# Optimization experiments

Measured on AMD Instinct MI355X. Metric: run time of the kernel, lower is better.

Reference implementation:

```python
import jax, jax.numpy as jnp
import numpy as np

B, T, N, F = 8, 12, 10000, 8
H = 64          # hidden_size
K = 2           # diffusion hops (gnn_kernel)
HOR = 12        # horizon
E = 320000      # num edges


def setup_inputs() -> dict:
    key = jax.random.key(0)
    ks = jax.random.split(key, 12)
    s = 0.1  # param scale
    return {
        "x": jax.random.normal(ks[0], (B, T, N, F), jnp.float32),
        "edge_index": jax.random.randint(ks[1], (2, E), 0, N, jnp.int64),
        "edge_weight": jax.random.uniform(ks[2], (E,), jnp.float32),
        "enc_W": jax.random.normal(ks[3], (F, H), jnp.float32) * s,
        "enc_b": jnp.zeros((H,), jnp.float32),
        "node_emb": jax.random.normal(ks[4], (N, H), jnp.float32) * s,
        "Wih": jax.random.normal(ks[5], (3 * H, H), jnp.float32) * s,
        "Whh": jax.random.normal(ks[6], (3 * H, H), jnp.float32) * s,
        "bih": jnp.zeros((3 * H,), jnp.float32),
        "bhh": jnp.zeros((3 * H,), jnp.float32),
        "filt_W": jax.random.normal(ks[7], (H * (2 * K + 1), H), jnp.float32) * s,
        "filt_b": jnp.zeros((H,), jnp.float32),
        "dec_W": jax.random.normal(ks[8], (H, F * HOR), jnp.float32) * s,
        "dec_b": jnp.zeros((F * HOR,), jnp.float32),
    }


def _gru_last(xs, Wih, Whh, bih, bhh):
    # xs: [T, M, H] -> last hidden state [M, H]; torch GRU gate order r,z,n
    gx = jnp.einsum('tmh,gh->tmg', xs, Wih) + bih  # [T, M, 3H]
    h0 = jnp.zeros(xs.shape[1:], xs.dtype)

    def step(h, gxt):
        gh = h @ Whh.T + bhh
        xr, xz, xn = jnp.split(gxt, 3, -1)
        hr, hz, hn = jnp.split(gh, 3, -1)
        r = jax.nn.sigmoid(xr + hr)
        z = jax.nn.sigmoid(xz + hz)
        n = jnp.tanh(xn + r * hn)
        return (1.0 - z) * n + z * h, None

    h, _ = jax.lax.scan(step, h0, gx)
    return h


def _diff_conv(h, edge_index, edge_weight, W, b):
    # h: [B, N, H]; diffusion conv with forward + backward transition matrices
    src, tgt = edge_index[0], edge_index[1]

    def prop(x, s, t, w):
        deg = jax.ops.segment_sum(w, t, num_segments=N)      # in-degree of aggregating node
        nw = w / jnp.where(deg[t] == 0, 1.0, deg[t])
        msg = x[:, s, :] * nw[None, :, None]                 # [B, E, H]
        return jnp.zeros_like(x).at[:, t].add(msg)

    outs = [h]  # root weight
    for s, t in ((src, tgt), (tgt, src)):  # forward then backward diffusion
        z = h
        for _ in range(K):
            z = prop(z, s, t, edge_weight)
            outs.append(z)
    return jnp.concatenate(outs, axis=-1) @ W + b


def reference(x, edge_index, edge_weight, enc_W, enc_b, node_emb, Wih, Whh,
              bih, bhh, filt_W, filt_b, dec_W, dec_b):
    x_enc = x @ enc_W + enc_b                         # [B,T,N,H]
    x_emb = x_enc + node_emb                          # broadcast over B,T
    xs = jnp.transpose(x_emb, (1, 0, 2, 3)).reshape(T, B * N, H)
    h = _gru_last(xs, Wih, Whh, bih, bhh).reshape(B, N, H)
    z = _diff_conv(h, edge_index, edge_weight, filt_W, filt_b)
    x_out = z @ dec_W + dec_b                         # [B,N,F*HOR]
    x_hor = x_out.reshape(B, N, HOR, F).transpose(0, 2, 1, 3)  # b t n f
    return x_hor
```

## Files before the change

### kernel.cpp

```cpp
#include <hip/hip_runtime.h>

typedef unsigned short ushort_t;

#define NN 10000
#define BB 8
#define TT 12
#define FF 8
#define HH 64
#define GG 192
#define HORZ 12
#define EE 320000
#define MM (BB*NN)

#define NL2E (-1.4426950408889634f)
#define P2L2E (2.8853900817779268f)

#define OFF_H    0u
#define OFF_F1   5120000u
#define OFF_F2   10240000u
#define OFF_B1   15360000u
#define OFF_B2   20480000u
#define OFF_BIAS 25600000u
#define OFF_W1   27520000u
#define OFF_DEGF 27521536u
#define OFF_DEGB 27531536u
#define OFF_CNTF 27541536u
#define OFF_CNTB 27551536u
#define OFF_PTRF 27561536u
#define OFF_PTRB 27571537u
#define OFF_EPKF 27581538u
#define OFF_EPKB 28221538u
#define OFF_FLAG 28861538u

typedef __attribute__((ext_vector_type(8))) short short8;
typedef __attribute__((ext_vector_type(4))) float f4v;

union I4S8 { int4 i; short8 s; };

__device__ __forceinline__ f4v mfma16(int4 a, int4 b, f4v c) {
    I4S8 ua, ub; ua.i = a; ub.i = b;
    return __builtin_amdgcn_mfma_f32_16x16x32_bf16(ua.s, ub.s, c, 0, 0, 0);
}

__device__ __forceinline__ unsigned f2bf_u(float f) {
    union { float f; unsigned u; } v; v.f = f;
    unsigned x = v.u;
    x += 0x7FFFu + ((x >> 16) & 1u);
    return x >> 16;
}
__device__ __forceinline__ int4 hi8(const float* f) {
    unsigned hb[8];
    #pragma unroll
    for (int i = 0; i < 8; i++) hb[i] = f2bf_u(f[i]);
    return make_int4((int)(hb[0]|(hb[1]<<16)), (int)(hb[2]|(hb[3]<<16)),
                     (int)(hb[4]|(hb[5]<<16)), (int)(hb[6]|(hb[7]<<16)));
}

__device__ __forceinline__ float f4c(const float4& v, int kk) {
    switch (kk) { case 0: return v.x; case 1: return v.y; case 2: return v.z; default: return v.w; }
}
#define FMA4(ACC, W, S) \
    ACC[0] = fmaf(S, W.x, ACC[0]); \
    ACC[1] = fmaf(S, W.y, ACC[1]); \
    ACC[2] = fmaf(S, W.z, ACC[2]); \
    ACC[3] = fmaf(S, W.w, ACC[3]);

__global__ void zero_k(float* p, int n) {
    int i = blockIdx.x * 256 + threadIdx.x;
    if (i < n) p[i] = 0.f;
}

__global__ void flag_k(const int* __restrict__ ei, int* flag) {
    if (threadIdx.x == 0 && blockIdx.x == 0) {
        int o = ei[1] | ei[3] | ei[5] | ei[7] | ei[9] | ei[11] | ei[13];
        flag[0] = (o == 0) ? 1 : 0;
    }
}

__device__ __forceinline__ void load_edge(const int* __restrict__ ei, int isI64,
                                          int e, int& s, int& t) {
    if (isI64) {
        const long long* p = (const long long*)ei;
        s = (int)p[e]; t = (int)p[EE + e];
    } else {
        s = ei[e]; t = ei[EE + e];
    }
}

__global__ void csr_count_k(const int* __restrict__ ei, const float* __restrict__ ew,
                            const int* __restrict__ flag,
                            int* cnt_f, int* cnt_b, float* deg_f, float* deg_b) {
    int e = blockIdx.x * 256 + threadIdx.x;
    if (e >= EE) return;
    int isI64 = flag[0];
    int s, t; load_edge(ei, isI64, e, s, t);
    if ((unsigned)s >= NN || (unsigned)t >= NN) return;
    float w = ew[e];
    atomicAdd(&cnt_f[t], 1); atomicAdd(&deg_f[t], w);
    atomicAdd(&cnt_b[s], 1); atomicAdd(&deg_b[s], w);
}

__global__ void scan_k(int* cnt_f, int* cnt_b, int* ptr_f, int* ptr_b) {
    int* cnt = blockIdx.x ? cnt_b : cnt_f;
    int* ptr = blockIdx.x ? ptr_b : ptr_f;
    __shared__ int part[256];
    int tid = threadIdx.x;
    const int CH = (NN + 255) / 256;
    int lo = tid * CH, hi = lo + CH; if (hi > NN) hi = NN; if (lo > NN) lo = NN;
    int s = 0;
    for (int i = lo; i < hi; i++) s += cnt[i];
    part[tid] = s;
    __syncthreads();
    if (tid == 0) {
        int run = 0;
        for (int i = 0; i < 256; i++) { int v = part[i]; part[i] = run; run += v; }
        ptr[NN] = run;
    }
    __syncthreads();
    int run = part[tid];
    for (int i = lo; i < hi; i++) { ptr[i] = run; run += cnt[i]; cnt[i] = 0; }
}

__global__ void csr_fill_k(const int* __restrict__ ei, const float* __restrict__ ew,
                           const int* __restrict__ flag,
                           const float* __restrict__ deg_f, const float* __restrict__ deg_b,
                           const int* __restrict__ ptr_f, const int* __restrict__ ptr_b,
                           int* cnt_f, int* cnt_b,
                           int* epk_f, int* epk_b) {
    int e = blockIdx.x * 256 + threadIdx.x;
    if (e >= EE) return;
    int isI64 = flag[0];
    int s, t; load_edge(ei, isI64, e, s, t);
    if ((unsigned)s >= NN || (unsigned)t >= NN) return;
    float w = ew[e];
    float df = deg_f[t];
    float nwf = w / ((df == 0.f) ? 1.f : df);
    int p = ptr_f[t] + atomicAdd(&cnt_f[t], 1);
    epk_f[2 * p] = s; epk_f[2 * p + 1] = __float_as_int(nwf);
    float db = deg_b[s];
    float nwb = w / ((db == 0.f) ? 1.f : db);
    int p2 = ptr_b[s] + atomicAdd(&cnt_b[s], 1);
    epk_b[2 * p2] = t; epk_b[2 * p2 + 1] = __float_as_int(nwb);
}

__global__ void w1_k(const float* __restrict__ encW, const float* __restrict__ wih,
                     float* __restrict__ W1) {
    int id = blockIdx.x * 256 + threadIdx.x;
    if (id >= FF * GG) return;
    int f = id / GG, g = id - f * GG;
    float acc = 0.f;
    for (int hh = 0; hh < HH; hh++)
        acc = fmaf(encW[f * HH + hh], wih[g * HH + hh], acc);
    W1[id] = acc * ((g < 128) ? NL2E : P2L2E);
}

__global__ __launch_bounds__(256, 2)
void biasA_k(const float* __restrict__ emb, const float* __restrict__ encb,
             const float* __restrict__ wih, const float* __restrict__ bih,
             const float* __restrict__ bhh, float* __restrict__ biasA) {
    __shared__ float wl[HH * GG];
    __shared__ float et[64 * 68];
    const int tid = threadIdx.x;
    const int n0 = blockIdx.x * 64;
    for (int idx = tid * 4; idx < GG * HH; idx += 1024) {
        float4 v = *(const float4*)&wih[idx];
        int g = idx >> 6, hh = idx & 63;
        wl[hh * GG + g] = v.x;
        wl[(hh + 1) * GG + g] = v.y;
        wl[(hh + 2) * GG + g] = v.z;
        wl[(hh + 3) * GG + g] = v.w;
    }
    {
        int row = tid >> 2, cc = (tid & 3) * 16;
        int n = n0 + row;
        #pragma unroll
        for (int u = 0; u < 4; u++) {
            float4 e4 = (n < NN) ? *(const float4*)&emb[(size_t)n * HH + cc + u * 4]
                                 : make_float4(0.f, 0.f, 0.f, 0.f);
            float4 b4 = *(const float4*)&encb[cc + u * 4];
            *(float4*)&et[row * 68 + cc + u * 4] =
                make_float4(e4.x + b4.x, e4.y + b4.y, e4.z + b4.z, e4.w + b4.w);
        }
    }
    __syncthreads();
    const int r0 = (tid >> 4) * 4;
    #pragma unroll 1
    for (int p = 0; p < 3; p++) {
        const int c0 = p * 64 + (tid & 15) * 4;
        float acc[4][4];
        float4 bi = *(const float4*)&bih[c0];
        float4 bh = (c0 < 128) ? *(const float4*)&bhh[c0] : make_float4(0.f, 0.f, 0.f, 0.f);
        #pragma unroll
        for (int i = 0; i < 4; i++) {
            acc[i][0] = bi.x + bh.x; acc[i][1] = bi.y + bh.y;
            acc[i][2] = bi.z + bh.z; acc[i][3] = bi.w + bh.w;
        }
        #pragma unroll 4
        for (int k4 = 0; k4 < 64; k4 += 4) {
            float4 hv[4];
            #pragma unroll
            for (int i = 0; i < 4; i++)
                hv[i] = *(const float4*)&et[(r0 + i) * 68 + k4];
            #pragma unroll
            for (int kk = 0; kk < 4; kk++) {
                const float4 wv = *(const float4*)&wl[(k4 + kk) * GG + c0];
                #pragma unroll
                for (int i = 0; i < 4; i++) {
                    float a_ = f4c(hv[i], kk);
                    FMA4(acc[i], wv, a_);
                }
            }
        }
        #pragma unroll
        for (int i = 0; i < 4; i++) {
            int n = n0 + r0 + i;
            if (n < NN)
                *(float4*)&biasA[(size_t)n * GG + c0] =
                    make_float4(acc[i][0], acc[i][1], acc[i][2], acc[i][3]);
        }
    }
}

__global__ __launch_bounds__(256, 2)
void gru_k(const float* __restrict__ x, const float* __restrict__ biasA,
           const float* __restrict__ W1, const float* __restrict__ whh,
           const float* __restrict__ bhh, float* __restrict__ h_out) {
    __shared__ int lds_B[24 * 64 * 4];
    __shared__ int lds_W1[12 * 64 * 4];
    __shared__ __align__(16) ushort_t lds_hb[4][16 * 68];

    const int tid = threadIdx.x;
    const int wave = tid >> 6, ln = tid & 63;
    const int quad = ln >> 4, lx = ln & 15;
    const int m0 = blockIdx.x * 64;
    ushort_t* hbw = (ushort_t*)lds_hb[wave];

    #pragma unroll
    for (int it = 0; it < 6; it++) {
        int slot = tid + it * 256;
        int fid = slot >> 6, l2 = slot & 63;
        int c = fid >> 1, q = fid & 1;
        int g = c * 16 + (l2 & 15);
        int k0 = q * 32 + ((l2 >> 4) & 3) * 8;
        float sc = (c < 8) ? NL2E : P2L2E;
        const float* wp = whh + (size_t)g * HH + k0;
        float4 v0 = *(const float4*)wp;
        float4 v1 = *(const float4*)(wp + 4);
        float fv[8] = {v0.x * sc, v0.y * sc, v0.z * sc, v0.w * sc,
                       v1.x * sc, v1.y * sc, v1.z * sc, v1.w * sc};
        *(int4*)&lds_B[slot * 4] = hi8(fv);
    }

    #pragma unroll
    for (int it = 0; it < 3; it++) {
        int slot = tid + it * 256;
        int f = slot >> 6, l2 = slot & 63;
        int4 v = make_int4(0, 0, 0, 0);
        if (l2 < 16) {
            int col = f * 16 + l2;
            float fv[8];
            #pragma unroll
            for (int k = 0; k < 8; k++) fv[k] = W1[k * GG + col];
            v = hi8(fv);
        }
        *(int4*)&lds_W1[slot * 4] = v;
    }

    f4v bR[4], bZ[4], bNx[4];
    float bHn[4];
    int rown[4];
    #pragma unroll
    for (int reg = 0; reg < 4; reg++) {
        int m = m0 + wave * 16 + quad * 4 + reg;
        int b = m / NN; rown[reg] = m - b * NN;
    }
    #pragma unroll
    for (int j = 0; j < 4; j++) {
        int c = j * 16 + lx;
        #pragma unroll
        for (int reg = 0; reg < 4; reg++) {
            const float* bp = biasA + (size_t)rown[reg] * GG;
            bR[j][reg]  = bp[c] * NL2E;
            bZ[j][reg]  = bp[64 + c] * NL2E;
            bNx[j][reg] = bp[128 + c] * P2L2E;
        }
        bHn[j] = bhh[128 + c] * P2L2E;
    }

    const float* xp = x;
    float4 xc0 = make_float4(0.f,0.f,0.f,0.f), xc1 = xc0;
    if (ln < 16) {
        int m = m0 + wave * 16 + ln;
        int b = m / NN; int n = m - b * NN;
        xp = x + ((size_t)(b * TT) * NN + n) * FF;
        xc0 = *(const float4*)xp;
        xc1 = *(const float4*)(xp + 4);
    }

    __syncthreads();

    f4v hp[4];
    #pragma unroll
    for (int j = 0; j < 4; j++) hp[j] = (f4v){0.f, 0.f, 0.f, 0.f};

    #pragma unroll 1
    for (int t = 0; t < TT; t++) {
        int4 axh = make_int4(0, 0, 0, 0);
        {
            float fv[8] = {xc0.x, xc0.y, xc0.z, xc0.w, xc1.x, xc1.y, xc1.z, xc1.w};
            if (ln < 16) axh = hi8(fv);
        }
        if (t < TT - 1 && ln < 16) {
            const float* xq = xp + (size_t)(t + 1) * (NN * FF);
            xc0 = *(const float4*)xq;
            xc1 = *(const float4*)(xq + 4);
        }

        int4 ahf[2];
        if (t) {
            const ushort_t* h0 = hbw + lx * 68 + quad * 8;
            long long a00, a01, a10, a11;
            __builtin_memcpy(&a00, h0, 8);
            __builtin_memcpy(&a01, h0 + 4, 8);
            __builtin_memcpy(&a10, h0 + 32, 8);
            __builtin_memcpy(&a11, h0 + 36, 8);
            ahf[0] = make_int4((int)a00, (int)(a00 >> 32), (int)a01, (int)(a01 >> 32));
            ahf[1] = make_int4((int)a10, (int)(a10 >> 32), (int)a11, (int)(a11 >> 32));
        }

        f4v accR[4], accZ[4], accNx[4], accNh[4];
        #pragma unroll
        for (int j = 0; j < 4; j++) {
            int4 wR = *(const int4*)&lds_W1[((j    ) * 64 + ln) * 4];
            int4 wZ = *(const int4*)&lds_W1[((j + 4) * 64 + ln) * 4];
            int4 wN = *(const int4*)&lds_W1[((j + 8) * 64 + ln) * 4];
            accR[j]  = mfma16(axh, wR, bR[j]);
            accZ[j]  = mfma16(axh, wZ, bZ[j]);
            accNx[j] = mfma16(axh, wN, bNx[j]);
            accNh[j] = (f4v){bHn[j], bHn[j], bHn[j], bHn[j]};
        }
        if (t) {
            #pragma unroll
            for (int j = 0; j < 4; j++) {
                #pragma unroll
                for (int q = 0; q < 2; q++) {
                    int4 bRf = *(const int4*)&lds_B[((j * 2 + q) * 64 + ln) * 4];
                    int4 bZf = *(const int4*)&lds_B[(((j + 4) * 2 + q) * 64 + ln) * 4];
                    int4 bNf = *(const int4*)&lds_B[(((j + 8) * 2 + q) * 64 + ln) * 4];
                    accR[j]  = mfma16(ahf[q], bRf, accR[j]);
                    accZ[j]  = mfma16(ahf[q], bZf, accZ[j]);
                    accNh[j] = mfma16(ahf[q], bNf, accNh[j]);
                }
            }
        }

        #pragma unroll
        for (int j = 0; j < 4; j++) {
            #pragma unroll
            for (int reg = 0; reg < 4; reg++) {
                float rr = __builtin_amdgcn_rcpf(1.f + __builtin_amdgcn_exp2f(accR[j][reg]));
                float zz = __builtin_amdgcn_rcpf(1.f + __builtin_amdgcn_exp2f(accZ[j][reg]));
                float pre = fmaf(rr, accNh[j][reg], accNx[j][reg]);
                float e2 = __builtin_amdgcn_exp2f(pre);
                float nn = fmaf(-2.f, __builtin_amdgcn_rcpf(e2 + 1.f), 1.f);
                float hv = fmaf(zz, hp[j][reg] - nn, nn);
                hp[j][reg] = hv;
                hbw[(quad * 4 + reg) * 68 + j * 16 + lx] = (ushort_t)f2bf_u(hv);
            }
        }
    }

    #pragma unroll
    for (int j = 0; j < 4; j++) {
        #pragma unroll
        for (int reg = 0; reg < 4; reg++) {
            int m = m0 + wave * 16 + quad * 4 + reg;
            h_out[(size_t)m * HH + j * 16 + lx] = hp[j][reg];
        }
    }
}

__global__ __launch_bounds__(128)
void prop_k(const float* __restrict__ srcF, float* __restrict__ dstF,
            const int* __restrict__ ptrF, const long long* __restrict__ epkF,
            const float* __restrict__ srcB, float* __restrict__ dstB,
            const int* __restrict__ ptrB, const long long* __restrict__ epkB) {
    const int wv = __builtin_amdgcn_readfirstlane(threadIdx.x >> 6);
    const int ln = threadIdx.x & 63;
    const int b = blockIdx.x & 7;
    const int node = (blockIdx.x >> 3) * 2 + wv;
    const float* src; float* dst; const int* ptr; const long long* ep;
    if (blockIdx.z == 0) { src = srcF; dst = dstF; ptr = ptrF; ep = epkF; }
    else                 { src = srcB; dst = dstB; ptr = ptrB; ep = epkB; }
    const int uoff = b * (NN * HH) + ln;
    const int e0 = ptr[node], e1 = ptr[node + 1];

    float a0 = 0.f, a1 = 0.f, a2 = 0.f, a3 = 0.f;
    float a4 = 0.f, a5 = 0.f, a6 = 0.f, a7 = 0.f;
    int j = e0;
    for (; j + 16 <= e1; j += 16) {
        long long r0 = ep[j + 0],  r1 = ep[j + 1],  r2 = ep[j + 2],  r3 = ep[j + 3];
        long long r4 = ep[j + 4],  r5 = ep[j + 5],  r6 = ep[j + 6],  r7 = ep[j + 7];
        long long r8 = ep[j + 8],  r9 = ep[j + 9],  rA = ep[j + 10], rB = ep[j + 11];
        long long rC = ep[j + 12], rD = ep[j + 13], rE = ep[j + 14], rF = ep[j + 15];
        float v0 = (src + ((size_t)(int)r0 << 6))[uoff];
        float v1 = (src + ((size_t)(int)r1 << 6))[uoff];
        float v2 = (src + ((size_t)(int)r2 << 6))[uoff];
        float v3 = (src + ((size_t)(int)r3 << 6))[uoff];
        float v4 = (src + ((size_t)(int)r4 << 6))[uoff];
        float v5 = (src + ((size_t)(int)r5 << 6))[uoff];
        float v6 = (src + ((size_t)(int)r6 << 6))[uoff];
        float v7 = (src + ((size_t)(int)r7 << 6))[uoff];
        float v8 = (src + ((size_t)(int)r8 << 6))[uoff];
        float v9 = (src + ((size_t)(int)r9 << 6))[uoff];
        float vA = (src + ((size_t)(int)rA << 6))[uoff];
        float vB = (src + ((size_t)(int)rB << 6))[uoff];
        float vC = (src + ((size_t)(int)rC << 6))[uoff];
        float vD = (src + ((size_t)(int)rD << 6))[uoff];
        float vE = (src + ((size_t)(int)rE << 6))[uoff];
        float vF = (src + ((size_t)(int)rF << 6))[uoff];
        a0 = fmaf(v0, __int_as_float((int)(r0 >> 32)), a0);
        a1 = fmaf(v1, __int_as_float((int)(r1 >> 32)), a1);
        a2 = fmaf(v2, __int_as_float((int)(r2 >> 32)), a2);
        a3 = fmaf(v3, __int_as_float((int)(r3 >> 32)), a3);
        a4 = fmaf(v4, __int_as_float((int)(r4 >> 32)), a4);
        a5 = fmaf(v5, __int_as_float((int)(r5 >> 32)), a5);
        a6 = fmaf(v6, __int_as_float((int)(r6 >> 32)), a6);
        a7 = fmaf(v7, __int_as_float((int)(r7 >> 32)), a7);
        a0 = fmaf(v8, __int_as_float((int)(r8 >> 32)), a0);
        a1 = fmaf(v9, __int_as_float((int)(r9 >> 32)), a1);
        a2 = fmaf(vA, __int_as_float((int)(rA >> 32)), a2);
        a3 = fmaf(vB, __int_as_float((int)(rB >> 32)), a3);
        a4 = fmaf(vC, __int_as_float((int)(rC >> 32)), a4);
        a5 = fmaf(vD, __int_as_float((int)(rD >> 32)), a5);
        a6 = fmaf(vE, __int_as_float((int)(rE >> 32)), a6);
        a7 = fmaf(vF, __int_as_float((int)(rF >> 32)), a7);
    }
    for (; j + 8 <= e1; j += 8) {
        long long r0 = ep[j + 0], r1 = ep[j + 1], r2 = ep[j + 2], r3 = ep[j + 3];
        long long r4 = ep[j + 4], r5 = ep[j + 5], r6 = ep[j + 6], r7 = ep[j + 7];
        float v0 = (src + ((size_t)(int)r0 << 6))[uoff];
        float v1 = (src + ((size_t)(int)r1 << 6))[uoff];
        float v2 = (src + ((size_t)(int)r2 << 6))[uoff];
        float v3 = (src + ((size_t)(int)r3 << 6))[uoff];
        float v4 = (src + ((size_t)(int)r4 << 6))[uoff];
        float v5 = (src + ((size_t)(int)r5 << 6))[uoff];
        float v6 = (src + ((size_t)(int)r6 << 6))[uoff];
        float v7 = (src + ((size_t)(int)r7 << 6))[uoff];
        a0 = fmaf(v0, __int_as_float((int)(r0 >> 32)), a0);
        a1 = fmaf(v1, __int_as_float((int)(r1 >> 32)), a1);
        a2 = fmaf(v2, __int_as_float((int)(r2 >> 32)), a2);
        a3 = fmaf(v3, __int_as_float((int)(r3 >> 32)), a3);
        a4 = fmaf(v4, __int_as_float((int)(r4 >> 32)), a4);
        a5 = fmaf(v5, __int_as_float((int)(r5 >> 32)), a5);
        a6 = fmaf(v6, __int_as_float((int)(r6 >> 32)), a6);
        a7 = fmaf(v7, __int_as_float((int)(r7 >> 32)), a7);
    }
    for (; j < e1; j++) {
        long long r0 = ep[j];
        a0 = fmaf((src + ((size_t)(int)r0 << 6))[uoff],
                  __int_as_float((int)(r0 >> 32)), a0);
    }
    float s = ((a0 + a1) + (a2 + a3)) + ((a4 + a5) + (a6 + a7));
    __builtin_nontemporal_store(s, &dst[((size_t)b * NN + node) * HH + ln]);
}

__global__ __launch_bounds__(256, 2)
void filtdec_k(const float* __restrict__ h, const float* __restrict__ f1,
               const float* __restrict__ f2, const float* __restrict__ b1,
               const float* __restrict__ b2,
               const float* __restrict__ filtW, const float* __restrict__ filtb,
               const float* __restrict__ decW, const float* __restrict__ decb,
               float* __restrict__ out) {
    __shared__ float lds_a[64 * 100];
    __shared__ float lds_w[64 * 100];
    const int tid = threadIdx.x;
    const int m0 = blockIdx.x * 64;
    const int c0 = (tid & 15) * 4, r0 = (tid >> 4) * 4;

    float acc[4][4];
    #pragma unroll
    for (int i = 0; i < 4; i++)
        #pragma unroll
        for (int j = 0; j < 4; j++) acc[i][j] = 0.f;

    #pragma unroll 1
    for (int q = 0; q < 5; q++) {
        const float* src = (q == 0) ? h : (q == 1) ? f1 : (q == 2) ? f2 : (q == 3) ? b1 : b2;
        {
            int row = tid >> 2, cc = (tid & 3) * 16;
            const float* sp = src + (size_t)(m0 + row) * HH + cc;
            float4 v0 = *(const float4*)(sp + 0);
            float4 v1 = *(const float4*)(sp + 4);
            float4 v2 = *(const float4*)(sp + 8);
            float4 v3 = *(const float4*)(sp + 12);
            *(float4*)&lds_a[row * 100 + cc + 0]  = v0;
            *(float4*)&lds_a[row * 100 + cc + 4]  = v1;
            *(float4*)&lds_a[row * 100 + cc + 8]  = v2;
            *(float4*)&lds_a[row * 100 + cc + 12] = v3;
        }
        {
            int k = tid >> 2, cc = (tid & 3) * 16;
            const float* wp = filtW + (size_t)(q * 64 + k) * HH + cc;
            float4 v0 = *(const float4*)(wp + 0);
            float4 v1 = *(const float4*)(wp + 4);
            float4 v2 = *(const float4*)(wp + 8);
            float4 v3 = *(const float4*)(wp + 12);
            *(float4*)&lds_w[k * 100 + cc + 0]  = v0;
            *(float4*)&lds_w[k * 100 + cc + 4]  = v1;
            *(float4*)&lds_w[k * 100 + cc + 8]  = v2;
            *(float4*)&lds_w[k * 100 + cc + 12] = v3;
        }
        __syncthreads();
        #pragma unroll 4
        for (int k4 = 0; k4 < 64; k4 += 4) {
            float4 iv[4];
            #pragma unroll
            for (int i = 0; i < 4; i++)
                iv[i] = *(const float4*)&lds_a[(r0 + i) * 100 + k4];
            #pragma unroll
            for (int kk = 0; kk < 4; kk++) {
                const float4 wv = *(const float4*)&lds_w[(k4 + kk) * 100 + c0];
                #pragma unroll
                for (int i = 0; i < 4; i++) {
                    float a_ = f4c(iv[i], kk);
                    FMA4(acc[i], wv, a_);
                }
            }
        }
        __syncthreads();
    }
    {
        float fb[4];
        #pragma unroll
        for (int j = 0; j < 4; j++) fb[j] = filtb[c0 + j];
        #pragma unroll
        for (int i = 0; i < 4; i++)
            *(float4*)&lds_a[(r0 + i) * 68 + c0] =
                make_float4(acc[i][0] + fb[0], acc[i][1] + fb[1],
                            acc[i][2] + fb[2], acc[i][3] + fb[3]);
    }
    {
        int k = tid >> 2, cc = (tid & 3) * 24;
        const float* wp = decW + k * 96 + cc;
        float* dstp = &lds_w[k * 100 + cc];
        #pragma unroll
        for (int u = 0; u < 6; u++) {
            float4 v = *(const float4*)(wp + u * 4);
            *(float4*)(dstp + u * 4) = v;
        }
    }
    __syncthreads();

    const int c0b = (tid & 15) * 6;
    float acc2[4][6];
    #pragma unroll
    for (int i = 0; i < 4; i++)
        #pragma unroll
        for (int j = 0; j < 6; j++) acc2[i][j] = 0.f;
    #pragma unroll 4
    for (int k4 = 0; k4 < 64; k4 += 4) {
        float4 zv[4];
        #pragma unroll
        for (int i = 0; i < 4; i++)
            zv[i] = *(const float4*)&lds_a[(r0 + i) * 68 + k4];
        #pragma unroll
        for (int kk = 0; kk < 4; kk++) {
            float2 wa = *(const float2*)&lds_w[(k4 + kk) * 100 + c0b];
            float2 wb = *(const float2*)&lds_w[(k4 + kk) * 100 + c0b + 2];
            float2 wc = *(const float2*)&lds_w[(k4 + kk) * 100 + c0b + 4];
            #pragma unroll
            for (int i = 0; i < 4; i++) {
                float zz = f4c(zv[i], kk);
                acc2[i][0] = fmaf(zz, wa.x, acc2[i][0]);
                acc2[i][1] = fmaf(zz, wa.y, acc2[i][1]);
                acc2[i][2] = fmaf(zz, wb.x, acc2[i][2]);
                acc2[i][3] = fmaf(zz, wb.y, acc2[i][3]);
                acc2[i][4] = fmaf(zz, wc.x, acc2[i][4]);
                acc2[i][5] = fmaf(zz, wc.y, acc2[i][5]);
            }
        }
    }
    __syncthreads();
    {
        float db[6];
        #pragma unroll
        for (int j = 0; j < 6; j++) db[j] = decb[c0b + j];
        #pragma unroll
        for (int i = 0; i < 4; i++)
            #pragma unroll
            for (int j = 0; j < 6; j++)
                lds_w[(r0 + i) * 100 + c0b + j] = acc2[i][j] + db[j];
    }
    __syncthreads();
    #pragma unroll 1
    for (int hor = 0; hor < HORZ; hor++) {
        int nl = tid >> 2, fp = tid & 3;
        int m = m0 + nl;
        int b = m / NN; int n = m - b * NN;
        float v0 = lds_w[nl * 100 + hor * 8 + 2 * fp];
        float v1 = lds_w[nl * 100 + hor * 8 + 2 * fp + 1];
        *(float2*)&out[(((size_t)b * HORZ + hor) * NN + n) * FF + 2 * fp] =
            make_float2(v0, v1);
    }
}

extern "C" void kernel_launch(void* const* d_in, const int* in_sizes, int n_in,
                              void* d_out, int out_size, void* d_ws, size_t ws_size,
                              hipStream_t stream) {
    (void)in_sizes; (void)n_in; (void)out_size; (void)ws_size;
    const float* x     = (const float*)d_in[0];
    const int*   ei    = (const int*)d_in[1];
    const float* ew    = (const float*)d_in[2];
    const float* encW  = (const float*)d_in[3];
    const float* encb  = (const float*)d_in[4];
    const float* emb   = (const float*)d_in[5];
    const float* wih   = (const float*)d_in[6];
    const float* whh   = (const float*)d_in[7];
    const float* bih   = (const float*)d_in[8];
    const float* bhh   = (const float*)d_in[9];
    const float* filtW = (const float*)d_in[10];
    const float* filtb = (const float*)d_in[11];
    const float* decW  = (const float*)d_in[12];
    const float* decb  = (const float*)d_in[13];
    float* out = (float*)d_out;

    float* ws = (float*)d_ws;
    float* h    = ws + OFF_H;
    float* f1   = ws + OFF_F1;
    float* f2   = ws + OFF_F2;
    float* b1   = ws + OFF_B1;
    float* b2   = ws + OFF_B2;
    float* bias = ws + OFF_BIAS;
    float* W1   = ws + OFF_W1;
    float* degf = ws + OFF_DEGF;
    float* degb = ws + OFF_DEGB;
    int* cntf = (int*)(ws + OFF_CNTF);
    int* cntb = (int*)(ws + OFF_CNTB);
    int* ptrf = (int*)(ws + OFF_PTRF);
    int* ptrb = (int*)(ws + OFF_PTRB);
    int* epkf = (int*)(ws + OFF_EPKF);
    int* epkb = (int*)(ws + OFF_EPKB);
    int* flag = (int*)(ws + OFF_FLAG);

    flag_k<<<1, 64, 0, stream>>>(ei, flag);
    zero_k<<<(40000 + 255) / 256, 256, 0, stream>>>(degf, 40000);
    csr_count_k<<<EE / 256, 256, 0, stream>>>(ei, ew, flag, cntf, cntb, degf, degb);
    scan_k<<<2, 256, 0, stream>>>(cntf, cntb, ptrf, ptrb);
    csr_fill_k<<<EE / 256, 256, 0, stream>>>(ei, ew, flag, degf, degb, ptrf, ptrb,
                                             cntf, cntb, epkf, epkb);
    w1_k<<<(FF * GG + 255) / 256, 256, 0, stream>>>(encW, wih, W1);
    biasA_k<<<(NN + 63) / 64, 256, 0, stream>>>(emb, encb, wih, bih, bhh, bias);
    gru_k<<<MM / 64, 256, 0, stream>>>(x, bias, W1, whh, bhh, h);
    {
        dim3 g((NN / 2) * BB, 1, 2);
        prop_k<<<g, 128, 0, stream>>>(h,  f1, ptrf, (const long long*)epkf,
                                      h,  b1, ptrb, (const long long*)epkb);
        prop_k<<<g, 128, 0, stream>>>(f1, f2, ptrf, (const long long*)epkf,
                                      b1, b2, ptrb, (const long long*)epkb);
    }
    filtdec_k<<<MM / 64, 256, 0, stream>>>(h, f1, f2, b1, b2,
                                           filtW, filtb, decW, decb, out);
}
```

Before: 512.6 us.

## Port filter and decoder GEMMs in filtdec_k to bf16 MFMA with split-precision activations

```diff
diff --git a/kernel.cpp b/kernel.cpp
--- a/kernel.cpp
+++ b/kernel.cpp
@@ -31,6 +31,8 @@
 #define OFF_EPKF 27581538u
 #define OFF_EPKB 28221538u
 #define OFF_FLAG 28861538u
+#define OFF_FWPK 28861540u
+#define OFF_DWPK 28871780u
 
 typedef __attribute__((ext_vector_type(8))) short short8;
 typedef __attribute__((ext_vector_type(4))) float f4v;
@@ -54,6 +56,19 @@
     for (int i = 0; i < 8; i++) hb[i] = f2bf_u(f[i]);
     return make_int4((int)(hb[0]|(hb[1]<<16)), (int)(hb[2]|(hb[3]<<16)),
                      (int)(hb[4]|(hb[5]<<16)), (int)(hb[6]|(hb[7]<<16)));
+}
+__device__ __forceinline__ void hilo8(const float* f, int4* ahi, int4* alo) {
+    unsigned hb[8];
+    float fl[8];
+    #pragma unroll
+    for (int i = 0; i < 8; i++) {
+        hb[i] = f2bf_u(f[i]);
+        union { unsigned u; float f; } hf; hf.u = hb[i] << 16;
+        fl[i] = f[i] - hf.f;
+    }
+    *ahi = make_int4((int)(hb[0]|(hb[1]<<16)), (int)(hb[2]|(hb[3]<<16)),
+                     (int)(hb[4]|(hb[5]<<16)), (int)(hb[6]|(hb[7]<<16)));
+    *alo = hi8(fl);
 }
 
 __device__ __forceinline__ float f4c(const float4& v, int kk) {
@@ -152,6 +167,29 @@
     for (int hh = 0; hh < HH; hh++)
         acc = fmaf(encW[f * HH + hh], wih[g * HH + hh], acc);
     W1[id] = acc * ((g < 128) ? NL2E : P2L2E);
+}
+
+__global__ void pack_k(const float* __restrict__ filtW, const float* __restrict__ decW,
+                       int* __restrict__ fwpk, int* __restrict__ dwpk) {
+    int id = blockIdx.x * 256 + threadIdx.x;
+    int ln = id & 63, set = id >> 6;
+    int quad = ln >> 4, lx = ln & 15;
+    if (set < 40) {
+        int ks = set >> 2, ct = set & 3;
+        float fv[8];
+        #pragma unroll
+        for (int j = 0; j < 8; j++)
+            fv[j] = filtW[(ks * 32 + quad * 8 + j) * 64 + ct * 16 + lx];
+        *(int4*)&fwpk[(set * 64 + ln) * 4] = hi8(fv);
+    } else if (set < 52) {
+        int s2 = set - 40;
+        int ks2 = s2 / 6, ct2 = s2 - ks2 * 6;
+        float fv[8];
+        #pragma unroll
+        for (int j = 0; j < 8; j++)
+            fv[j] = decW[(ks2 * 32 + quad * 8 + j) * 96 + ct2 * 16 + lx];
+        *(int4*)&dwpk[(s2 * 64 + ln) * 4] = hi8(fv);
+    }
 }
 
 __global__ __launch_bounds__(256, 2)
@@ -465,143 +503,91 @@
     __builtin_nontemporal_store(s, &dst[((size_t)b * NN + node) * HH + ln]);
 }
 
-__global__ __launch_bounds__(256, 2)
+__global__ __launch_bounds__(256)
 void filtdec_k(const float* __restrict__ h, const float* __restrict__ f1,
                const float* __restrict__ f2, const float* __restrict__ b1,
                const float* __restrict__ b2,
-               const float* __restrict__ filtW, const float* __restrict__ filtb,
-               const float* __restrict__ decW, const float* __restrict__ decb,
+               const int4* __restrict__ fwpk, const float* __restrict__ filtb,
+               const int4* __restrict__ dwpk, const float* __restrict__ decb,
                float* __restrict__ out) {
-    __shared__ float lds_a[64 * 100];
-    __shared__ float lds_w[64 * 100];
+    __shared__ __align__(16) ushort_t lds_z[4][16 * 68];
     const int tid = threadIdx.x;
+    const int wave = tid >> 6, ln = tid & 63;
+    const int quad = ln >> 4, lx = ln & 15;
     const int m0 = blockIdx.x * 64;
-    const int c0 = (tid & 15) * 4, r0 = (tid >> 4) * 4;
-
-    float acc[4][4];
-    #pragma unroll
-    for (int i = 0; i < 4; i++)
-        #pragma unroll
-        for (int j = 0; j < 4; j++) acc[i][j] = 0.f;
+    const int arow = m0 + wave * 16 + lx;
+    ushort_t* zb = (ushort_t*)lds_z[wave];
+
+    f4v zacc[4];
+    #pragma unroll
+    for (int ct = 0; ct < 4; ct++) {
+        float fb = filtb[ct * 16 + lx];
+        zacc[ct] = (f4v){fb, fb, fb, fb};
+    }
 
     #pragma unroll 1
     for (int q = 0; q < 5; q++) {
         const float* src = (q == 0) ? h : (q == 1) ? f1 : (q == 2) ? f2 : (q == 3) ? b1 : b2;
-        {
-            int row = tid >> 2, cc = (tid & 3) * 16;
-            const float* sp = src + (size_t)(m0 + row) * HH + cc;
-            float4 v0 = *(const float4*)(sp + 0);
-            float4 v1 = *(const float4*)(sp + 4);
-            float4 v2 = *(const float4*)(sp + 8);
-            float4 v3 = *(const float4*)(sp + 12);
-            *(float4*)&lds_a[row * 100 + cc + 0]  = v0;
-            *(float4*)&lds_a[row * 100 + cc + 4]  = v1;
-            *(float4*)&lds_a[row * 100 + cc + 8]  = v2;
-            *(float4*)&lds_a[row * 100 + cc + 12] = v3;
-        }
-        {
-            int k = tid >> 2, cc = (tid & 3) * 16;
-            const float* wp = filtW + (size_t)(q * 64 + k) * HH + cc;
-            float4 v0 = *(const float4*)(wp + 0);
-            float4 v1 = *(const float4*)(wp + 4);
-            float4 v2 = *(const float4*)(wp + 8);
-            float4 v3 = *(const float4*)(wp + 12);
-            *(float4*)&lds_w[k * 100 + cc + 0]  = v0;
-            *(float4*)&lds_w[k * 100 + cc + 4]  = v1;
-            *(float4*)&lds_w[k * 100 + cc + 8]  = v2;
-            *(float4*)&lds_w[k * 100 + cc + 12] = v3;
-        }
-        __syncthreads();
-        #pragma unroll 4
-        for (int k4 = 0; k4 < 64; k4 += 4) {
-            float4 iv[4];
+        const float* rp = src + (size_t)arow * HH + quad * 8;
+        #pragma unroll
+        for (int half = 0; half < 2; half++) {
+            float4 v0 = *(const float4*)(rp + half * 32);
+            float4 v1 = *(const float4*)(rp + half * 32 + 4);
+            float fv[8] = {v0.x, v0.y, v0.z, v0.w, v1.x, v1.y, v1.z, v1.w};
+            int4 ahi, alo;
+            hilo8(fv, &ahi, &alo);
+            int ks = q * 2 + half;
             #pragma unroll
-            for (int i = 0; i < 4; i++)
-                iv[i] = *(const float4*)&lds_a[(r0 + i) * 100 + k4];
-            #pragma unroll
-            for (int kk = 0; kk < 4; kk++) {
-                const float4 wv = *(const float4*)&lds_w[(k4 + kk) * 100 + c0];
-                #pragma unroll
-                for (int i = 0; i < 4; i++) {
-                    float a_ = f4c(iv[i], kk);
-                    FMA4(acc[i], wv, a_);
-                }
+            for (int ct = 0; ct < 4; ct++) {
+                int4 bf = fwpk[(ks * 4 + ct) * 64 + ln];
+                zacc[ct] = mfma16(ahi, bf, zacc[ct]);
+                zacc[ct] = mfma16(alo, bf, zacc[ct]);
             }
         }
-        __syncthreads();
-    }
+    }
+
+    #pragma unroll
+    for (int ct = 0; ct < 4; ct++)
+        #pragma unroll
+        for (int reg = 0; reg < 4; reg++)
+            zb[(quad * 4 + reg) * 68 + ct * 16 + lx] = (ushort_t)f2bf_u(zacc[ct][reg]);
+
+    int4 ahf[2];
     {
-        float fb[4];
-        #pragma unroll
-        for (int j = 0; j < 4; j++) fb[j] = filtb[c0 + j];
-        #pragma unroll
-        for (int i = 0; i < 4; i++)
-            *(float4*)&lds_a[(r0 + i) * 68 + c0] =
-                make_float4(acc[i][0] + fb[0], acc[i][1] + fb[1],
-                            acc[i][2] + fb[2], acc[i][3] + fb[3]);
-    }
-    {
-        int k = tid >> 2, cc = (tid & 3) * 24;
-        const float* wp = decW + k * 96 + cc;
-        float* dstp = &lds_w[k * 100 + cc];
-        #pragma unroll
-        for (int u = 0; u < 6; u++) {
-            float4 v = *(const float4*)(wp + u * 4);
-            *(float4*)(dstp + u * 4) = v;
-        }
-    }
-    __syncthreads();
-
-    const int c0b = (tid & 15) * 6;
-    float acc2[4][6];
-    #pragma unroll
-    for (int i = 0; i < 4; i++)
-        #pragma unroll
-        for (int j = 0; j < 6; j++) acc2[i][j] = 0.f;
-    #pragma unroll 4
-    for (int k4 = 0; k4 < 64; k4 += 4) {
-        float4 zv[4];
-        #pragma unroll
-        for (int i = 0; i < 4; i++)
-            zv[i] = *(const float4*)&lds_a[(r0 + i) * 68 + k4];
-        #pragma unroll
-        for (int kk = 0; kk < 4; kk++) {
-            float2 wa = *(const float2*)&lds_w[(k4 + kk) * 100 + c0b];
-            float2 wb = *(const float2*)&lds_w[(k4 + kk) * 100 + c0b + 2];
-            float2 wc = *(const float2*)&lds_w[(k4 + kk) * 100 + c0b + 4];
-            #pragma unroll
-            for (int i = 0; i < 4; i++) {
-                float zz = f4c(zv[i], kk);
-                acc2[i][0] = fmaf(zz, wa.x, acc2[i][0]);
-                acc2[i][1] = fmaf(zz, wa.y, acc2[i][1]);
-                acc2[i][2] = fmaf(zz, wb.x, acc2[i][2]);
-                acc2[i][3] = fmaf(zz, wb.y, acc2[i][3]);
-                acc2[i][4] = fmaf(zz, wc.x, acc2[i][4]);
-                acc2[i][5] = fmaf(zz, wc.y, acc2[i][5]);
-            }
-        }
-    }
-    __syncthreads();
-    {
-        float db[6];
-        #pragma unroll
-        for (int j = 0; j < 6; j++) db[j] = decb[c0b + j];
-        #pragma unroll
-        for (int i = 0; i < 4; i++)
-            #pragma unroll
-            for (int j = 0; j < 6; j++)
-                lds_w[(r0 + i) * 100 + c0b + j] = acc2[i][j] + db[j];
-    }
-    __syncthreads();
-    #pragma unroll 1
-    for (int hor = 0; hor < HORZ; hor++) {
-        int nl = tid >> 2, fp = tid & 3;
-        int m = m0 + nl;
-        int b = m / NN; int n = m - b * NN;
-        float v0 = lds_w[nl * 100 + hor * 8 + 2 * fp];
-        float v1 = lds_w[nl * 100 + hor * 8 + 2 * fp + 1];
-        *(float2*)&out[(((size_t)b * HORZ + hor) * NN + n) * FF + 2 * fp] =
-            make_float2(v0, v1);
+        const ushort_t* z0 = zb + lx * 68 + quad * 8;
+        long long a00, a01, a10, a11;
+        __builtin_memcpy(&a00, z0, 8);
+        __builtin_memcpy(&a01, z0 + 4, 8);
+        __builtin_memcpy(&a10, z0 + 32, 8);
+        __builtin_memcpy(&a11, z0 + 36, 8);
+        ahf[0] = make_int4((int)a00, (int)(a00 >> 32), (int)a01, (int)(a01 >> 32));
+        ahf[1] = make_int4((int)a10, (int)(a10 >> 32), (int)a11, (int)(a11 >> 32));
+    }
+
+    f4v oacc[6];
+    #pragma unroll
+    for (int ct2 = 0; ct2 < 6; ct2++) {
+        float db = decb[ct2 * 16 + lx];
+        oacc[ct2] = (f4v){db, db, db, db};
+    }
+    #pragma unroll
+    for (int ks2 = 0; ks2 < 2; ks2++)
+        #pragma unroll
+        for (int ct2 = 0; ct2 < 6; ct2++) {
+            int4 bf = dwpk[(ks2 * 6 + ct2) * 64 + ln];
+            oacc[ct2] = mfma16(ahf[ks2], bf, oacc[ct2]);
+        }
+
+    #pragma unroll
+    for (int ct2 = 0; ct2 < 6; ct2++) {
+        int col = ct2 * 16 + lx;
+        int hor = col >> 3, f = col & 7;
+        #pragma unroll
+        for (int reg = 0; reg < 4; reg++) {
+            int m = m0 + wave * 16 + quad * 4 + reg;
+            int b = m / NN; int n = m - b * NN;
+            out[(((size_t)b * HORZ + hor) * NN + n) * FF + f] = oacc[ct2][reg];
+        }
     }
 }
 
@@ -642,6 +628,8 @@
     int* epkf = (int*)(ws + OFF_EPKF);
     int* epkb = (int*)(ws + OFF_EPKB);
     int* flag = (int*)(ws + OFF_FLAG);
+    int* fwpk = (int*)(ws + OFF_FWPK);
+    int* dwpk = (int*)(ws + OFF_DWPK);
 
     flag_k<<<1, 64, 0, stream>>>(ei, flag);
     zero_k<<<(40000 + 255) / 256, 256, 0, stream>>>(degf, 40000);
@@ -650,6 +638,7 @@
     csr_fill_k<<<EE / 256, 256, 0, stream>>>(ei, ew, flag, degf, degb, ptrf, ptrb,
                                              cntf, cntb, epkf, epkb);
     w1_k<<<(FF * GG + 255) / 256, 256, 0, stream>>>(encW, wih, W1);
+    pack_k<<<13, 256, 0, stream>>>(filtW, decW, fwpk, dwpk);
     biasA_k<<<(NN + 63) / 64, 256, 0, stream>>>(emb, encb, wih, bih, bhh, bias);
     gru_k<<<MM / 64, 256, 0, stream>>>(x, bias, W1, whh, bhh, h);
     {
@@ -660,5 +649,6 @@
                                       b1, b2, ptrb, (const long long*)epkb);
     }
     filtdec_k<<<MM / 64, 256, 0, stream>>>(h, f1, f2, b1, b2,
-                                           filtW, filtb, decW, decb, out);
-}
+                                           (const int4*)fwpk, filtb,
+                                           (const int4*)dwpk, decb, out);
+}
```

Result: faster. 476.3 us (-7.1%).
